# Kernel optimization log

Hardware: AMD Instinct MI355X
Metric: run time of the kernel (lower is better)

The kernel has to match this reference:

```python
import jax, jax.numpy as jnp
import numpy as np

N_NODES = 100000
N_EDGES = 3200000
N_GRAPHS = 256
FEAT = 128
HIDDEN = 128
N_CLASSES = 10


def setup_inputs() -> dict:
    key = jax.random.key(0)
    ks = jax.random.split(key, 12)
    x = jax.random.normal(ks[0], (N_NODES, FEAT), dtype=jnp.float32)
    edge_index = jax.random.randint(ks[1], (2, N_EDGES), 0, N_NODES, dtype=jnp.int64)
    batch = jnp.sort(jax.random.randint(ks[2], (N_NODES,), 0, N_GRAPHS, dtype=jnp.int64))
    s = 0.05
    return {
        "x": x,
        "edge_index": edge_index,
        "batch": batch,
        "W1": jax.random.normal(ks[3], (FEAT, HIDDEN), dtype=jnp.float32) * s,
        "b1": jnp.zeros((HIDDEN,), dtype=jnp.float32),
        "W2": jax.random.normal(ks[4], (HIDDEN, HIDDEN), dtype=jnp.float32) * s,
        "b2": jnp.zeros((HIDDEN,), dtype=jnp.float32),
        "W3": jax.random.normal(ks[5], (HIDDEN, HIDDEN), dtype=jnp.float32) * s,
        "b3": jnp.zeros((HIDDEN,), dtype=jnp.float32),
        "lin1_w": jax.random.normal(ks[6], (HIDDEN, HIDDEN), dtype=jnp.float32) * s,
        "lin1_b": jnp.zeros((HIDDEN,), dtype=jnp.float32),
        "lin2_w": jax.random.normal(ks[7], (HIDDEN, N_CLASSES), dtype=jnp.float32) * s,
        "lin2_b": jnp.zeros((N_CLASSES,), dtype=jnp.float32),
    }


def _gcn_norm(edge_index, n_nodes):
    # PyG GCNConv default: add self-loops, symmetric normalization.
    src = jnp.concatenate([edge_index[0], jnp.arange(n_nodes, dtype=edge_index.dtype)])
    dst = jnp.concatenate([edge_index[1], jnp.arange(n_nodes, dtype=edge_index.dtype)])
    deg = jax.ops.segment_sum(jnp.ones_like(dst, dtype=jnp.float32), dst, num_segments=n_nodes)
    dis = jnp.where(deg > 0, jax.lax.rsqrt(jnp.maximum(deg, 1.0)), 0.0)
    norm = dis[src] * dis[dst]  # [E + N]
    return src, dst, norm


def _gcn_conv(x, src, dst, norm, W, b, n_nodes):
    h = x @ W                               # [N, H]
    msg = h[src] * norm[:, None]            # gather + scale, [E+N, H]
    out = jax.ops.segment_sum(msg, dst, num_segments=n_nodes)  # scatter-add
    return out + b


def reference(x, edge_index, batch, W1, b1, W2, b2, W3, b3, lin1_w, lin1_b, lin2_w, lin2_b):
    n = x.shape[0]
    src, dst, norm = _gcn_norm(edge_index, n)
    h = jax.nn.relu(_gcn_conv(x, src, dst, norm, W1, b1, n))
    h = jax.nn.relu(_gcn_conv(h, src, dst, norm, W2, b2, n))
    h = jax.nn.relu(_gcn_conv(h, src, dst, norm, W3, b3, n))
    # global mean pool over graphs
    sums = jax.ops.segment_sum(h, batch, num_segments=N_GRAPHS)
    cnts = jax.ops.segment_sum(jnp.ones((n,), dtype=h.dtype), batch, num_segments=N_GRAPHS)
    g = sums / jnp.maximum(cnts, 1.0)[:, None]
    g = jax.nn.relu(g @ lin1_w + lin1_b)
    # dropout p=0.5 is identity at inference
    return g @ lin2_w + lin2_b
```

## Files before the change

### kernel.cpp

```cpp
#include <hip/hip_runtime.h>
#include <hip/hip_fp16.h>

#define FEAT 128
#define CHUNK 8192
#define BSH 7
#define CAP 6144
#define RSTRIDE 784

#define QS  16.0f
#define QSI 0.0625f

typedef _Float16 half8 __attribute__((ext_vector_type(8)));
typedef float floatx4 __attribute__((ext_vector_type(4)));
typedef float floatx2 __attribute__((ext_vector_type(2)));

__device__ __forceinline__ unsigned int enc8x4(float a, float b, float c, float d) {
  unsigned int r = __builtin_amdgcn_cvt_pk_fp8_f32(a, b, 0u, false);
  return __builtin_amdgcn_cvt_pk_fp8_f32(c, d, r, true);
}
__device__ __forceinline__ void acc8(unsigned int w, float* a) {
  floatx2 v0 = __builtin_amdgcn_cvt_pk_f32_fp8(w, false);
  floatx2 v1 = __builtin_amdgcn_cvt_pk_f32_fp8(w, true);
  a[0] += v0.x; a[1] += v0.y; a[2] += v1.x; a[3] += v1.y;
}


__global__ __launch_bounds__(256) void sort_prep_kernel(
    const int* __restrict__ ei, int E, int nchunks, int nbuk,
    int* __restrict__ pairs, int* __restrict__ runs,
    const float* __restrict__ W1, const float* __restrict__ W2,
    const float* __restrict__ W3, _Float16* __restrict__ P1,
    _Float16* __restrict__ P2, _Float16* __restrict__ P3,
    unsigned char* __restrict__ qA, unsigned char* __restrict__ qB, int N) {
  __shared__ int lhist[1024];
  __shared__ int lofs[1024];
  __shared__ int lcur[1024];
  __shared__ int tsum[256];
  __shared__ int stage[CHUNK];
  int t = threadIdx.x;
  if ((int)blockIdx.x >= nchunks) {
    int b = blockIdx.x - nchunks;
    if (b == 24) {
      if (t < 16) ((unsigned long long*)(qA + (size_t)N * FEAT))[t] = 0ull;
      else if (t < 32) ((unsigned long long*)(qB + (size_t)N * FEAT))[t - 16] = 0ull;
      return;
    }
    const float* W = (b < 8) ? W1 : (b < 16) ? W2 : W3;
    _Float16* P = (b < 8) ? P1 : (b < 16) ? P2 : P3;
    int e = (b & 7) * 256 + t;
    int l = e & 63;
    int ks = (e >> 6) & 3;
    int tn = e >> 8;
    int n = tn * 16 + (l & 15);
    int k0 = ks * 32 + (l >> 4) * 8;
    half8 v;
#pragma unroll
    for (int j = 0; j < 8; ++j) v[j] = (_Float16)W[(k0 + j) * 128 + n];
    *(half8*)(P + (size_t)e * 8) = v;
    return;
  }
  int c = blockIdx.x;
  int e0 = c * CHUNK;
  int e1 = e0 + CHUNK; if (e1 > E) e1 = E;
  int cnt = e1 - e0;
#pragma unroll
  for (int u = 0; u < 4; ++u) lhist[t + u * 256] = 0;
  __syncthreads();
  for (int j = e0 + t; j < e1; j += 256) atomicAdd(&lhist[ei[E + j] >> BSH], 1);
  __syncthreads();
  int a0 = lhist[4 * t], a1 = lhist[4 * t + 1];
  int a2 = lhist[4 * t + 2], a3 = lhist[4 * t + 3];
  int s = ((a0 + a1) + (a2 + a3));
  tsum[t] = s;
  __syncthreads();
  for (int o = 1; o < 256; o <<= 1) {
    int x = (t >= o) ? tsum[t - o] : 0;
    __syncthreads();
    tsum[t] += x;
    __syncthreads();
  }
  int base = tsum[t] - s;
  lofs[4 * t] = base;       lcur[4 * t] = base;
  lofs[4 * t + 1] = base + a0;           lcur[4 * t + 1] = base + a0;
  lofs[4 * t + 2] = base + a0 + a1;      lcur[4 * t + 2] = base + a0 + a1;
  lofs[4 * t + 3] = base + a0 + a1 + a2; lcur[4 * t + 3] = base + a0 + a1 + a2;
  __syncthreads();
  for (int k = t; k < nbuk; k += 256) runs[(size_t)c * RSTRIDE + k] = lofs[k];
  if (t == 0) runs[(size_t)c * RSTRIDE + nbuk] = cnt;
  for (int j = e0 + t; j < e1; j += 256) {
    int sv = ei[j];
    int d = ei[E + j];
    int p = atomicAdd(&lcur[d >> BSH], 1);
    stage[p] = sv | ((d & 127) << 24);
  }
  __syncthreads();
  for (int j = t; j < cnt; j += 256) pairs[e0 + j] = stage[j];
}

__global__ __launch_bounds__(256) void bucket_csr_kernel(
    const int* __restrict__ pairs, const int* __restrict__ runs, int nchunks,
    int nbuk, int2* __restrict__ row_se, float* __restrict__ dis,
    int* __restrict__ col, int N) {
  __shared__ int rs[512], rl[512], ro[512];
  __shared__ int cnt[128], sc[128];
  __shared__ int stage[CAP];
  int b = blockIdx.x, t = threadIdx.x;
  for (int c = t; c < 512; c += 256) {
    int s0 = 0, len = 0;
    if (c < nchunks) {
      const int* rr = runs + (size_t)c * RSTRIDE;
      s0 = rr[b];
      len = rr[b + 1] - s0;
    }
    rs[c] = s0; rl[c] = len;
  }
  if (t < 128) cnt[t] = 0;
  __syncthreads();
  ro[t] = rl[t]; ro[t + 256] = rl[t + 256];
  __syncthreads();
  for (int o = 1; o < 512; o <<= 1) {
    int v0 = (t >= o) ? ro[t - o] : 0;
    int v1 = (t + 256 >= o) ? ro[t + 256 - o] : 0;
    __syncthreads();
    ro[t] += v0; ro[t + 256] += v1;
    __syncthreads();
  }
  int ce = ro[511];
  int y0 = ro[t] - rl[t];
  int y1 = ro[t + 256] - rl[t + 256];
  __syncthreads();
  ro[t] = y0; ro[t + 256] = y1;
  __syncthreads();
  int colbase = b * CAP;
  bool fits = ce <= CAP;
  if (fits) {
    for (int c = t; c < nchunks; c += 256) {
      int gs = c * CHUNK + rs[c];
      int base = ro[c];
      int len = rl[c];
      for (int j = 0; j < len; ++j) {
        int p = pairs[gs + j];
        stage[base + j] = p;
        atomicAdd(&cnt[((unsigned)p) >> 24], 1);
      }
    }
  } else {
    for (int c = t; c < nchunks; c += 256) {
      int gs = c * CHUNK + rs[c];
      for (int j = 0; j < rl[c]; ++j)
        atomicAdd(&cnt[((unsigned)pairs[gs + j]) >> 24], 1);
    }
  }
  __syncthreads();
  int v = 0, excl = 0;
  if (t < 128) { v = cnt[t]; sc[t] = v; }
  __syncthreads();
  for (int o = 1; o < 128; o <<= 1) {
    int x = (t >= o && t < 128) ? sc[t - o] : 0;
    __syncthreads();
    if (t < 128) sc[t] += x;
    __syncthreads();
  }
  if (t < 128) {
    excl = sc[t] - v;
    int node = b * 128 + t;
    if (node < N) {
      row_se[node] = make_int2(colbase + excl, colbase + excl + v);
      dis[node] = rsqrtf((float)(v + 1));
    }
    cnt[t] = excl;
  }
  __syncthreads();
  if (fits) {
    for (int j = t; j < ce; j += 256) {
      int p = stage[j];
      int loc = atomicAdd(&cnt[((unsigned)p) >> 24], 1);
      col[colbase + loc] = (p & 0xFFFFFF) << 7;
    }
  } else {
    for (int c = t; c < nchunks; c += 256) {
      int gs = c * CHUNK + rs[c];
      for (int j = 0; j < rl[c]; ++j) {
        int p = pairs[gs + j];
        int loc = atomicAdd(&cnt[((unsigned)p) >> 24], 1);
        if (loc < CAP) col[colbase + loc] = (p & 0xFFFFFF) << 7;
      }
    }
  }
}


__global__ __launch_bounds__(256) void mm1_kernel(
    const float* __restrict__ Av, const _Float16* __restrict__ Wpk,
    const float* __restrict__ scale, unsigned char* __restrict__ C, int N) {
  int t = threadIdx.x;
  int wave = t >> 6, lane = t & 63;
  int quad = lane >> 4, nidx = lane & 15;
  int m0 = blockIdx.x * 64 + wave * 16;
  int arow = m0 + nidx;
  bool avalid = arow < N;
  floatx4 acc[8];
#pragma unroll
  for (int tn = 0; tn < 8; ++tn) acc[tn] = (floatx4){0.f, 0.f, 0.f, 0.f};
#pragma unroll
  for (int ks = 0; ks < 4; ++ks) {
    half8 x = {};
    if (avalid) {
      const float* p = Av + (size_t)arow * 128 + ks * 32 + quad * 8;
      float4 f0 = *(const float4*)p;
      float4 f1 = *(const float4*)(p + 4);
      x[0] = (_Float16)f0.x; x[1] = (_Float16)f0.y;
      x[2] = (_Float16)f0.z; x[3] = (_Float16)f0.w;
      x[4] = (_Float16)f1.x; x[5] = (_Float16)f1.y;
      x[6] = (_Float16)f1.z; x[7] = (_Float16)f1.w;
    }
#pragma unroll
    for (int tn = 0; tn < 8; ++tn) {
      half8 wfrag = *(const half8*)(Wpk + ((size_t)((tn * 4 + ks) * 64 + lane)) * 8);
      acc[tn] = __builtin_amdgcn_mfma_f32_16x16x32_f16(wfrag, x, acc[tn], 0, 0, 0);
    }
  }
  if (avalid) {
    float s = scale[arow] * QS;
#pragma unroll
    for (int tn = 0; tn < 8; ++tn) {
      unsigned int r = enc8x4(acc[tn][0] * s, acc[tn][1] * s,
                              acc[tn][2] * s, acc[tn][3] * s);
      *(unsigned int*)(C + (size_t)arow * 128 + tn * 16 + quad * 4) = r;
    }
  }
}

__global__ __launch_bounds__(256) void agg_fuse_kernel(
    const unsigned char* __restrict__ hs_in, const int2* __restrict__ row_se,
    const int* __restrict__ col, const float* __restrict__ dis,
    const float* __restrict__ bias, const _Float16* __restrict__ Wpk,
    unsigned char* __restrict__ hs_out, int N) {
  __shared__ _Float16 Xs[16][136];
  int t = threadIdx.x;
  int wave = t >> 6, lane = t & 63;
  int lin = lane & 15;
  int nl = wave * 4 + (lane >> 4);
  int node = blockIdx.x * 16 + nl;
  bool valid = node < N;
  int lin8 = lin * 8;
  int zoff = N << 7;
  float a[8] = {0.f, 0.f, 0.f, 0.f, 0.f, 0.f, 0.f, 0.f};
  int selfoff = (valid ? (node << 7) : zoff) + lin8;
  uint2 s0 = *(const uint2*)(hs_in + (unsigned)selfoff);
  acc8(s0.x, a); acc8(s0.y, a + 4);
  int2 se = valid ? row_se[node] : make_int2(0, 0);
  int i = se.x, e = se.y;
  while (__any(i < e)) {
#pragma unroll
    for (int u = 0; u < 16; ++u) {
      int idx = i + u;
      int off = (idx < e) ? col[idx] : zoff;
      uint2 r = *(const uint2*)(hs_in + (unsigned)(off + lin8));
      acc8(r.x, a); acc8(r.y, a + 4);
    }
    i += 16;
  }
  float d = valid ? dis[node] * QSI : 0.f;
  const float* bp = bias + lin8;
  half8 hx;
#pragma unroll
  for (int j = 0; j < 8; ++j) {
    float o = valid ? fmaxf(fmaf(d, a[j], bp[j]), 0.f) : 0.f;
    hx[j] = (_Float16)o;
  }
  *(half8*)&Xs[nl][lin8] = hx;
  __syncthreads();
  int quad = lane >> 4, nidx = lane & 15;
  floatx4 acc0 = (floatx4){0.f, 0.f, 0.f, 0.f};
  floatx4 acc1 = (floatx4){0.f, 0.f, 0.f, 0.f};
  int tn0 = wave * 2;
#pragma unroll
  for (int ks = 0; ks < 4; ++ks) {
    half8 x = *(const half8*)&Xs[nidx][ks * 32 + quad * 8];
    half8 w0 = *(const half8*)(Wpk + ((size_t)((tn0 * 4 + ks) * 64 + lane)) * 8);
    half8 w1 = *(const half8*)(Wpk + ((size_t)(((tn0 + 1) * 4 + ks) * 64 + lane)) * 8);
    acc0 = __builtin_amdgcn_mfma_f32_16x16x32_f16(w0, x, acc0, 0, 0, 0);
    acc1 = __builtin_amdgcn_mfma_f32_16x16x32_f16(w1, x, acc1, 0, 0, 0);
  }
  int onode = blockIdx.x * 16 + nidx;
  if (onode < N) {
    float sc = dis[onode] * QS;
    unsigned int r0 = enc8x4(acc0[0] * sc, acc0[1] * sc, acc0[2] * sc, acc0[3] * sc);
    *(unsigned int*)(hs_out + (size_t)onode * 128 + tn0 * 16 + quad * 4) = r0;
    unsigned int r1 = enc8x4(acc1[0] * sc, acc1[1] * sc, acc1[2] * sc, acc1[3] * sc);
    *(unsigned int*)(hs_out + (size_t)onode * 128 + (tn0 + 1) * 16 + quad * 4) = r1;
  }
}

__global__ __launch_bounds__(256) void agg_kernel(
    const unsigned char* __restrict__ hs, const int2* __restrict__ row_se,
    const int* __restrict__ col, const float* __restrict__ dis,
    const float* __restrict__ bias, _Float16* __restrict__ out, int N) {
  int t = threadIdx.x;
  int wave = t >> 6, lane = t & 63;
  int lin = lane & 15;
  int nl = wave * 4 + (lane >> 4);
  int node = blockIdx.x * 16 + nl;
  bool valid = node < N;
  int lin8 = lin * 8;
  int zoff = N << 7;
  float a[8] = {0.f, 0.f, 0.f, 0.f, 0.f, 0.f, 0.f, 0.f};
  int selfoff = (valid ? (node << 7) : zoff) + lin8;
  uint2 s0 = *(const uint2*)(hs + (unsigned)selfoff);
  acc8(s0.x, a); acc8(s0.y, a + 4);
  int2 se = valid ? row_se[node] : make_int2(0, 0);
  int i = se.x, e = se.y;
  while (__any(i < e)) {
#pragma unroll
    for (int u = 0; u < 16; ++u) {
      int idx = i + u;
      int off = (idx < e) ? col[idx] : zoff;
      uint2 r = *(const uint2*)(hs + (unsigned)(off + lin8));
      acc8(r.x, a); acc8(r.y, a + 4);
    }
    i += 16;
  }
  if (valid) {
    float d = dis[node] * QSI;
    const float* bp = bias + lin8;
    half8 hx;
#pragma unroll
    for (int j = 0; j < 8; ++j)
      hx[j] = (_Float16)fmaxf(fmaf(d, a[j], bp[j]), 0.f);
    *(half8*)(out + (size_t)node * FEAT + lin8) = hx;
  }
}

__global__ __launch_bounds__(128) void head_kernel(
    const __half* __restrict__ h, const int* __restrict__ batch,
    const float* __restrict__ l1w, const float* __restrict__ l1b,
    const float* __restrict__ l2w, const float* __restrict__ l2b,
    float* __restrict__ out, int N, int C) {
  __shared__ float row[128];
  __shared__ float row2[128];
  int grp = blockIdx.x, t = threadIdx.x;
  int lo = 0, hi = N;
  while (lo < hi) { int m = (lo + hi) >> 1; if (batch[m] < grp) lo = m + 1; else hi = m; }
  int start = lo;
  hi = N;
  while (lo < hi) { int m = (lo + hi) >> 1; if (batch[m] <= grp) lo = m + 1; else hi = m; }
  int end = lo;
  float a0 = 0.f, a1 = 0.f, a2 = 0.f, a3 = 0.f;
  int i = start;
  for (; i + 4 <= end; i += 4) {
    a0 += __half2float(h[(size_t)i * 128 + t]);
    a1 += __half2float(h[(size_t)(i + 1) * 128 + t]);
    a2 += __half2float(h[(size_t)(i + 2) * 128 + t]);
    a3 += __half2float(h[(size_t)(i + 3) * 128 + t]);
  }
  for (; i < end; ++i) a0 += __half2float(h[(size_t)i * 128 + t]);
  float sum = (a0 + a1) + (a2 + a3);
  float cntf = (float)(end - start);
  row[t] = sum / fmaxf(cntf, 1.0f);
  __syncthreads();
  float acc = l1b[t];
#pragma unroll 8
  for (int k = 0; k < 128; ++k) acc = fmaf(row[k], l1w[k * 128 + t], acc);
  row2[t] = fmaxf(acc, 0.f);
  __syncthreads();
  if (t < C) {
    float a = l2b[t];
#pragma unroll 8
    for (int k = 0; k < 128; ++k) a = fmaf(row2[k], l2w[k * C + t], a);
    out[grp * C + t] = a;
  }
}


extern "C" void kernel_launch(void* const* d_in, const int* in_sizes, int n_in,
                              void* d_out, int out_size, void* d_ws, size_t ws_size,
                              hipStream_t stream) {
  const float* x   = (const float*)d_in[0];
  const int*   ei  = (const int*)d_in[1];
  const int*   bat = (const int*)d_in[2];
  const float* W1  = (const float*)d_in[3];
  const float* b1  = (const float*)d_in[4];
  const float* W2  = (const float*)d_in[5];
  const float* b2  = (const float*)d_in[6];
  const float* W3  = (const float*)d_in[7];
  const float* b3  = (const float*)d_in[8];
  const float* l1w = (const float*)d_in[9];
  const float* l1b = (const float*)d_in[10];
  const float* l2w = (const float*)d_in[11];
  const float* l2b = (const float*)d_in[12];

  int N = in_sizes[2];
  int E = in_sizes[1] / 2;
  int C = in_sizes[12];
  int G = out_size / C;
  float* outp = (float*)d_out;

  char* wp = (char*)d_ws;
  auto alloc = [&](size_t bytes) -> void* {
    void* p = (void*)wp;
    wp += (bytes + 255) & ~(size_t)255;
    return p;
  };
  int nbuk    = (N + 127) / 128;
  int nchunks = (E + CHUNK - 1) / CHUNK;

  float*    dis    = (float*)alloc((size_t)N * 4);
  int2*     row_se = (int2*)alloc((size_t)N * 8);
  int*      col    = (int*)alloc((size_t)nbuk * CAP * 4);
  int*      pairs  = (int*)alloc((size_t)nchunks * CHUNK * 4);
  int*      runs   = (int*)alloc((size_t)nchunks * RSTRIDE * 4);
  _Float16* Wpk1   = (_Float16*)alloc(16384 * 2);
  _Float16* Wpk2   = (_Float16*)alloc(16384 * 2);
  _Float16* Wpk3   = (_Float16*)alloc(16384 * 2);
  unsigned char* qA = (unsigned char*)alloc((size_t)(N + 1) * FEAT);
  unsigned char* qB = (unsigned char*)alloc((size_t)(N + 1) * FEAT);
  _Float16* hout  = (_Float16*)alloc((size_t)N * FEAT * 2);

  sort_prep_kernel<<<nchunks + 25, 256, 0, stream>>>(
      ei, E, nchunks, nbuk, pairs, runs, W1, W2, W3, Wpk1, Wpk2, Wpk3,
      qA, qB, N);
  bucket_csr_kernel<<<nbuk, 256, 0, stream>>>(pairs, runs, nchunks, nbuk,
                                              row_se, dis, col, N);

  int mmB = (N + 63) / 64;
  int fB  = (N + 15) / 16;

  mm1_kernel<<<mmB, 256, 0, stream>>>(x, Wpk1, dis, qA, N);
  agg_fuse_kernel<<<fB, 256, 0, stream>>>(qA, row_se, col, dis, b1,
                                          Wpk2, qB, N);
  agg_fuse_kernel<<<fB, 256, 0, stream>>>(qB, row_se, col, dis, b2,
                                          Wpk3, qA, N);
  agg_kernel<<<fB, 256, 0, stream>>>(qA, row_se, col, dis, b3, hout, N);
  head_kernel<<<G, 128, 0, stream>>>((const __half*)hout, bat, l1w, l1b,
                                     l2w, l2b, outp, N, C);
}
```

Baseline: 525.9 us.

## Widen per-lane gather to 16 bytes and process 32 nodes per block

Each aggregation lane now gathers 16 FP8 features with uint4 loads, so 8 lanes cover a node row and a 256-thread block handles 32 nodes instead of 16. The inner neighbor loop is split into separate phases that load column indices, issue all 8 row gathers, then accumulate, which exposes more loads in flight. In the fused kernel each wave now computes 4 output tiles for one 16-node tile, so each W fragment load feeds twice as many nodes. The cost is higher register pressure from 16 accumulators and 8 uint4 buffers, and fewer, larger blocks.

```diff
diff --git a/kernel.cpp b/kernel.cpp
--- a/kernel.cpp
+++ b/kernel.cpp
@@ -236,60 +236,78 @@
     const int* __restrict__ col, const float* __restrict__ dis,
     const float* __restrict__ bias, const _Float16* __restrict__ Wpk,
     unsigned char* __restrict__ hs_out, int N) {
-  __shared__ _Float16 Xs[16][136];
+  __shared__ _Float16 Xs[32][136];
   int t = threadIdx.x;
   int wave = t >> 6, lane = t & 63;
-  int lin = lane & 15;
-  int nl = wave * 4 + (lane >> 4);
-  int node = blockIdx.x * 16 + nl;
+  int lin = lane & 7;
+  int nl = wave * 8 + (lane >> 3);
+  int node = blockIdx.x * 32 + nl;
   bool valid = node < N;
-  int lin8 = lin * 8;
+  int lin16 = lin * 16;
   int zoff = N << 7;
-  float a[8] = {0.f, 0.f, 0.f, 0.f, 0.f, 0.f, 0.f, 0.f};
-  int selfoff = (valid ? (node << 7) : zoff) + lin8;
-  uint2 s0 = *(const uint2*)(hs_in + (unsigned)selfoff);
-  acc8(s0.x, a); acc8(s0.y, a + 4);
+  float a[16];
+#pragma unroll
+  for (int j = 0; j < 16; ++j) a[j] = 0.f;
+  int selfoff = (valid ? (node << 7) : zoff) + lin16;
+  uint4 s0 = *(const uint4*)(hs_in + (unsigned)selfoff);
+  acc8(s0.x, a); acc8(s0.y, a + 4); acc8(s0.z, a + 8); acc8(s0.w, a + 12);
   int2 se = valid ? row_se[node] : make_int2(0, 0);
   int i = se.x, e = se.y;
   while (__any(i < e)) {
-#pragma unroll
-    for (int u = 0; u < 16; ++u) {
+    int c[8];
+#pragma unroll
+    for (int u = 0; u < 8; ++u) {
       int idx = i + u;
-      int off = (idx < e) ? col[idx] : zoff;
-      uint2 r = *(const uint2*)(hs_in + (unsigned)(off + lin8));
-      acc8(r.x, a); acc8(r.y, a + 4);
-    }
-    i += 16;
+      c[u] = (idx < e) ? col[idx] : zoff;
+    }
+    uint4 r[8];
+#pragma unroll
+    for (int u = 0; u < 8; ++u)
+      r[u] = *(const uint4*)(hs_in + (unsigned)(c[u] + lin16));
+#pragma unroll
+    for (int u = 0; u < 8; ++u) {
+      acc8(r[u].x, a);     acc8(r[u].y, a + 4);
+      acc8(r[u].z, a + 8); acc8(r[u].w, a + 12);
+    }
+    i += 8;
   }
   float d = valid ? dis[node] * QSI : 0.f;
-  const float* bp = bias + lin8;
-  half8 hx;
+  const float* bp = bias + lin16;
+  half8 hx0, hx1;
 #pragma unroll
   for (int j = 0; j < 8; ++j) {
-    float o = valid ? fmaxf(fmaf(d, a[j], bp[j]), 0.f) : 0.f;
-    hx[j] = (_Float16)o;
-  }
-  *(half8*)&Xs[nl][lin8] = hx;
+    float o0 = valid ? fmaxf(fmaf(d, a[j], bp[j]), 0.f) : 0.f;
+    float o1 = valid ? fmaxf(fmaf(d, a[j + 8], bp[j + 8]), 0.f) : 0.f;
+    hx0[j] = (_Float16)o0;
+    hx1[j] = (_Float16)o1;
+  }
+  *(half8*)&Xs[nl][lin16] = hx0;
+  *(half8*)&Xs[nl][lin16 + 8] = hx1;
   __syncthreads();
   int quad = lane >> 4, nidx = lane & 15;
-  floatx4 acc0 = (floatx4){0.f, 0.f, 0.f, 0.f};
-  floatx4 acc1 = (floatx4){0.f, 0.f, 0.f, 0.f};
-  int tn0 = wave * 2;
+  int ntile = wave >> 1;
+  int f0 = (wave & 1) * 4;
+  floatx4 acc[4];
+#pragma unroll
+  for (int f = 0; f < 4; ++f) acc[f] = (floatx4){0.f, 0.f, 0.f, 0.f};
 #pragma unroll
   for (int ks = 0; ks < 4; ++ks) {
-    half8 x = *(const half8*)&Xs[nidx][ks * 32 + quad * 8];
-    half8 w0 = *(const half8*)(Wpk + ((size_t)((tn0 * 4 + ks) * 64 + lane)) * 8);
-    half8 w1 = *(const half8*)(Wpk + ((size_t)(((tn0 + 1) * 4 + ks) * 64 + lane)) * 8);
-    acc0 = __builtin_amdgcn_mfma_f32_16x16x32_f16(w0, x, acc0, 0, 0, 0);
-    acc1 = __builtin_amdgcn_mfma_f32_16x16x32_f16(w1, x, acc1, 0, 0, 0);
-  }
-  int onode = blockIdx.x * 16 + nidx;
+    half8 x = *(const half8*)&Xs[ntile * 16 + nidx][ks * 32 + quad * 8];
+#pragma unroll
+    for (int f = 0; f < 4; ++f) {
+      half8 wf = *(const half8*)(Wpk + ((size_t)(((f0 + f) * 4 + ks) * 64 + lane)) * 8);
+      acc[f] = __builtin_amdgcn_mfma_f32_16x16x32_f16(wf, x, acc[f], 0, 0, 0);
+    }
+  }
+  int onode = blockIdx.x * 32 + ntile * 16 + nidx;
   if (onode < N) {
     float sc = dis[onode] * QS;
-    unsigned int r0 = enc8x4(acc0[0] * sc, acc0[1] * sc, acc0[2] * sc, acc0[3] * sc);
-    *(unsigned int*)(hs_out + (size_t)onode * 128 + tn0 * 16 + quad * 4) = r0;
-    unsigned int r1 = enc8x4(acc1[0] * sc, acc1[1] * sc, acc1[2] * sc, acc1[3] * sc);
-    *(unsigned int*)(hs_out + (size_t)onode * 128 + (tn0 + 1) * 16 + quad * 4) = r1;
+#pragma unroll
+    for (int f = 0; f < 4; ++f) {
+      unsigned int rq = enc8x4(acc[f][0] * sc, acc[f][1] * sc,
+                               acc[f][2] * sc, acc[f][3] * sc);
+      *(unsigned int*)(hs_out + (size_t)onode * 128 + (f0 + f) * 16 + quad * 4) = rq;
+    }
   }
 }
 
@@ -299,36 +317,49 @@
     const float* __restrict__ bias, _Float16* __restrict__ out, int N) {
   int t = threadIdx.x;
   int wave = t >> 6, lane = t & 63;
-  int lin = lane & 15;
-  int nl = wave * 4 + (lane >> 4);
-  int node = blockIdx.x * 16 + nl;
+  int lin = lane & 7;
+  int nl = wave * 8 + (lane >> 3);
+  int node = blockIdx.x * 32 + nl;
   bool valid = node < N;
-  int lin8 = lin * 8;
+  int lin16 = lin * 16;
   int zoff = N << 7;
-  float a[8] = {0.f, 0.f, 0.f, 0.f, 0.f, 0.f, 0.f, 0.f};
-  int selfoff = (valid ? (node << 7) : zoff) + lin8;
-  uint2 s0 = *(const uint2*)(hs + (unsigned)selfoff);
-  acc8(s0.x, a); acc8(s0.y, a + 4);
+  float a[16];
+#pragma unroll
+  for (int j = 0; j < 16; ++j) a[j] = 0.f;
+  int selfoff = (valid ? (node << 7) : zoff) + lin16;
+  uint4 s0 = *(const uint4*)(hs + (unsigned)selfoff);
+  acc8(s0.x, a); acc8(s0.y, a + 4); acc8(s0.z, a + 8); acc8(s0.w, a + 12);
   int2 se = valid ? row_se[node] : make_int2(0, 0);
   int i = se.x, e = se.y;
   while (__any(i < e)) {
-#pragma unroll
-    for (int u = 0; u < 16; ++u) {
+    int c[8];
+#pragma unroll
+    for (int u = 0; u < 8; ++u) {
       int idx = i + u;
-      int off = (idx < e) ? col[idx] : zoff;
-      uint2 r = *(const uint2*)(hs + (unsigned)(off + lin8));
-      acc8(r.x, a); acc8(r.y, a + 4);
-    }
-    i += 16;
+      c[u] = (idx < e) ? col[idx] : zoff;
+    }
+    uint4 r[8];
+#pragma unroll
+    for (int u = 0; u < 8; ++u)
+      r[u] = *(const uint4*)(hs + (unsigned)(c[u] + lin16));
+#pragma unroll
+    for (int u = 0; u < 8; ++u) {
+      acc8(r[u].x, a);     acc8(r[u].y, a + 4);
+      acc8(r[u].z, a + 8); acc8(r[u].w, a + 12);
+    }
+    i += 8;
   }
   if (valid) {
     float d = dis[node] * QSI;
-    const float* bp = bias + lin8;
-    half8 hx;
-#pragma unroll
-    for (int j = 0; j < 8; ++j)
-      hx[j] = (_Float16)fmaxf(fmaf(d, a[j], bp[j]), 0.f);
-    *(half8*)(out + (size_t)node * FEAT + lin8) = hx;
+    const float* bp = bias + lin16;
+    half8 hx0, hx1;
+#pragma unroll
+    for (int j = 0; j < 8; ++j) {
+      hx0[j] = (_Float16)fmaxf(fmaf(d, a[j], bp[j]), 0.f);
+      hx1[j] = (_Float16)fmaxf(fmaf(d, a[j + 8], bp[j + 8]), 0.f);
+    }
+    *(half8*)(out + (size_t)node * FEAT + lin16) = hx0;
+    *(half8*)(out + (size_t)node * FEAT + lin16 + 8) = hx1;
   }
 }
 
@@ -424,14 +455,14 @@
                                               row_se, dis, col, N);
 
   int mmB = (N + 63) / 64;
-  int fB  = (N + 15) / 16;
+  int gB  = (N + 31) / 32;
 
   mm1_kernel<<<mmB, 256, 0, stream>>>(x, Wpk1, dis, qA, N);
-  agg_fuse_kernel<<<fB, 256, 0, stream>>>(qA, row_se, col, dis, b1,
+  agg_fuse_kernel<<<gB, 256, 0, stream>>>(qA, row_se, col, dis, b1,
                                           Wpk2, qB, N);
-  agg_fuse_kernel<<<fB, 256, 0, stream>>>(qB, row_se, col, dis, b2,
+  agg_fuse_kernel<<<gB, 256, 0, stream>>>(qB, row_se, col, dis, b2,
                                           Wpk3, qA, N);
-  agg_kernel<<<fB, 256, 0, stream>>>(qA, row_se, col, dis, b3, hout, N);
+  agg_kernel<<<gB, 256, 0, stream>>>(qA, row_se, col, dis, b3, hout, N);
   head_kernel<<<G, 128, 0, stream>>>((const __half*)hout, bat, l1w, l1b,
                                      l2w, l2b, outp, N, C);
 }
```

New measurement: 470.0 us. 10.6% less time.
